# Optimization experiments

Measured on AMD Instinct MI355X. Metric: run time of the kernel, lower is better.

## Reference

```python
import jax, jax.numpy as jnp
import numpy as np
from jax import lax

B, C, H, W = 2, 256, 200, 336
N_ROI = 512
NUM_CLASSES = 81


def setup_inputs() -> dict:
    key = jax.random.key(0)
    ks = jax.random.split(key, 20)
    feat = jax.random.normal(ks[0], (B, C, H, W), dtype=jnp.float32)
    # proposals in feature-map coordinates, x1<x2, y1<y2
    x1 = jax.random.uniform(ks[1], (N_ROI,)) * (0.7 * W)
    y1 = jax.random.uniform(ks[2], (N_ROI,)) * (0.7 * H)
    x2 = jnp.minimum(x1 + 8.0 + jax.random.uniform(ks[3], (N_ROI,)) * (0.29 * W), W - 1.0)
    y2 = jnp.minimum(y1 + 8.0 + jax.random.uniform(ks[4], (N_ROI,)) * (0.29 * H), H - 1.0)
    boxes = jnp.stack([x1, y1, x2, y2], axis=1).astype(jnp.float32)
    batch_idx = jax.random.randint(ks[5], (N_ROI,), 0, B)
    s = 0.02
    def rn(k, shape):
        return s * jax.random.normal(k, shape, dtype=jnp.float32)
    d_in = C * 7 * 7  # 12544
    return {
        'feat': feat, 'boxes': boxes,
        'bw1': rn(ks[6], (d_in, 1024)), 'bw2': rn(ks[7], (1024, 1024)), 'bwo': rn(ks[8], (1024, 4 * NUM_CLASSES)),
        'cw1': rn(ks[9], (d_in, 1024)), 'cw2': rn(ks[10], (1024, 1024)), 'cwo': rn(ks[11], (1024, NUM_CLASSES)),
        'm1': rn(ks[12], (C, C, 3, 3)), 'm2': rn(ks[13], (C, C, 3, 3)),
        'm3': rn(ks[14], (C, C, 3, 3)), 'm4': rn(ks[15], (C, C, 3, 3)),
        'mdc': rn(ks[16], (C, C, 2, 2)),  # IOHW for conv_transpose
        'mpr': rn(ks[17], (NUM_CLASSES, C, 1, 1)),
        'batch_idx': batch_idx,
    }


def roi_align(feat, boxes, batch_idx, out_size, sampling_ratio=2):
    """Bilinear RoIAlign. feat [B,C,H,W], boxes [N,4] (x1,y1,x2,y2) in feature coords.
    Returns [N,C,out_size,out_size]."""
    N = boxes.shape[0]
    _, Cc, Hh, Ww = feat.shape
    P = out_size * sampling_ratio
    x1, y1, x2, y2 = boxes[:, 0], boxes[:, 1], boxes[:, 2], boxes[:, 3]
    steps = (jnp.arange(P, dtype=feat.dtype) + 0.5) / P  # [P]
    xs = jnp.clip(x1[:, None] + steps[None, :] * (x2 - x1)[:, None], 0.0, Ww - 1.0)  # [N,P]
    ys = jnp.clip(y1[:, None] + steps[None, :] * (y2 - y1)[:, None], 0.0, Hh - 1.0)  # [N,P]
    x0 = jnp.floor(xs).astype(jnp.int32); x1i = jnp.minimum(x0 + 1, Ww - 1); lx = xs - x0
    y0 = jnp.floor(ys).astype(jnp.int32); y1i = jnp.minimum(y0 + 1, Hh - 1); ly = ys - y0
    b = batch_idx[:, None, None]                   # [N,1,1]
    yy0, yy1 = y0[:, :, None], y1i[:, :, None]     # [N,P,1]
    xx0, xx1 = x0[:, None, :], x1i[:, None, :]     # [N,1,P]
    # gathers -> [N,P,P,C] (advanced indices first, channel slice last)
    f00 = feat[b, :, yy0, xx0]
    f01 = feat[b, :, yy0, xx1]
    f10 = feat[b, :, yy1, xx0]
    f11 = feat[b, :, yy1, xx1]
    wy = ly[:, :, None, None]  # [N,P,1,1]
    wx = lx[:, None, :, None]  # [N,1,P,1]
    val = (f00 * (1 - wy) * (1 - wx) + f01 * (1 - wy) * wx
           + f10 * wy * (1 - wx) + f11 * wy * wx)  # [N,P,P,C]
    pooled = val.reshape(N, out_size, sampling_ratio, out_size, sampling_ratio, Cc).mean(axis=(2, 4))
    return pooled.transpose(0, 3, 1, 2)  # [N,C,out,out]


def _conv(x, w, pad='SAME'):
    return lax.conv_general_dilated(x, w, (1, 1), pad,
                                    dimension_numbers=('NCHW', 'OIHW', 'NCHW'))


def reference(feat, boxes, bw1, bw2, bwo, cw1, cw2, cwo,
              m1, m2, m3, m4, mdc, mpr, batch_idx):
    # RoIAlign (post-NMS proposals) -> box / cls / mask heads
    r7 = roi_align(feat, boxes, batch_idx, 7, 2)          # [N,C,7,7]
    flat = r7.reshape(r7.shape[0], -1)                    # [N, C*49]
    box_result = jax.nn.relu(jax.nn.relu(flat @ bw1) @ bw2) @ bwo   # [N, 4*classes]
    cls_result = jax.nn.relu(jax.nn.relu(flat @ cw1) @ cw2) @ cwo   # [N, classes]
    x = roi_align(feat, boxes, batch_idx, 14, 2)          # [N,C,14,14]
    for w in (m1, m2, m3, m4):
        x = jax.nn.relu(_conv(x, w))
    x = jax.nn.relu(lax.conv_transpose(x, mdc, (2, 2), 'VALID',
                                       dimension_numbers=('NCHW', 'IOHW', 'NCHW')))  # [N,C,28,28]
    mask_result = _conv(x, mpr)                           # [N, classes, 28, 28]
    return (box_result, cls_result, mask_result)
```

## Files before the change

### kernel.cpp

```cpp
#include <hip/hip_runtime.h>
#include <stdint.h>

#define BB 2
#define CC 256
#define HH 200
#define WW 336
#define NROI 512
#define NCLS 81

typedef __attribute__((ext_vector_type(8))) short bf16x8;
typedef __attribute__((ext_vector_type(4))) float f32x4;

__device__ inline unsigned short f2bf(float f) {
  unsigned int u = __builtin_bit_cast(unsigned int, f);
  u += 0x7fffu + ((u >> 16) & 1u);
  return (unsigned short)(u >> 16);
}
__device__ inline float bf2f(unsigned short h) {
  unsigned int u = ((unsigned int)h) << 16;
  return __builtin_bit_cast(float, u);
}

__device__ inline void gl_lds(const void* gp, void* lp) {
  __builtin_amdgcn_global_load_lds(
      (const __attribute__((address_space(1))) unsigned int*)gp,
      (__attribute__((address_space(3))) unsigned int*)lp, 16, 0, 0);
}

__global__ void k_nchw2nhwc(const float* __restrict__ src, unsigned short* __restrict__ dst) {
  __shared__ float t[32][33];
  int b = blockIdx.z;
  int p0 = blockIdx.x * 32;
  int c0 = blockIdx.y * 32;
  int tx = threadIdx.x & 31, ty = threadIdx.x >> 5;
  const float* s = src + (size_t)b * CC * HH * WW;
  unsigned short* d = dst + (size_t)b * CC * HH * WW;
#pragma unroll
  for (int q = 0; q < 4; ++q)
    t[ty + q * 8][tx] = s[(size_t)(c0 + ty + q * 8) * (HH * WW) + p0 + tx];
  __syncthreads();
#pragma unroll
  for (int q = 0; q < 4; ++q)
    d[(size_t)(p0 + ty + q * 8) * CC + c0 + tx] = f2bf(t[tx][ty + q * 8]);
}

__global__ void k_repack_convw4(const float* __restrict__ w0, const float* __restrict__ w1,
                                const float* __restrict__ w2, const float* __restrict__ w3,
                                unsigned short* __restrict__ wT) {
  int d = blockIdx.x * 256 + threadIdx.x;
  if (d >= 589824) return;
  int which = blockIdx.y;
  const float* w = (which == 0) ? w0 : (which == 1) ? w1 : (which == 2) ? w2 : w3;
  int c = d & 255, o = (d >> 8) & 255, t = d >> 16;
  wT[(size_t)which * 589824 + d] = f2bf(w[o * 2304 + c * 9 + t]);
}

__global__ void k_repack_deconv(const float* __restrict__ mdc, unsigned short* __restrict__ wd) {
  int d = blockIdx.x * 256 + threadIdx.x;
  if (d >= 262144) return;
  int c = d & 255, o = (d >> 8) & 255, tap = d >> 16;
  int r = tap >> 1, s = tap & 1;
  wd[d] = f2bf(mdc[c * 1024 + o * 4 + (1 - r) * 2 + (1 - s)]);
}

__global__ void k_repack_mpr(const float* __restrict__ mpr, unsigned short* __restrict__ mT) {
  int d = blockIdx.x * 256 + threadIdx.x;
  if (d >= 32768) return;
  int c = d & 255, o = d >> 8;
  mT[d] = (o < 81) ? f2bf(mpr[o * 256 + c]) : (unsigned short)0;
}

__global__ void k_repack_w1(const float* __restrict__ src, unsigned short* __restrict__ dst) {
  __shared__ float t[32][33];
  int s = blockIdx.x;
  int c0 = blockIdx.y * 32;
  int n0 = blockIdx.z * 32;
  int tx = threadIdx.x & 31, ty = threadIdx.x >> 5;
#pragma unroll
  for (int q = 0; q < 4; ++q)
    t[ty + q * 8][tx] = src[(size_t)((c0 + ty + q * 8) * 49 + s) * 1024 + n0 + tx];
  __syncthreads();
#pragma unroll
  for (int q = 0; q < 4; ++q)
    dst[(size_t)(n0 + ty + q * 8) * 12544 + s * 256 + c0 + tx] = f2bf(t[tx][ty + q * 8]);
}

__global__ void k_transpose_w(const float* __restrict__ src, unsigned short* __restrict__ dst,
                              int K, int Nreal, int Nphys) {
  __shared__ float t[32][33];
  int k0 = blockIdx.x * 32;
  int n0 = blockIdx.y * 32;
  int tx = threadIdx.x & 31, ty = threadIdx.x >> 5;
#pragma unroll
  for (int q = 0; q < 4; ++q) {
    int n = n0 + tx;
    t[ty + q * 8][tx] = (n < Nreal) ? src[(size_t)(k0 + ty + q * 8) * Nreal + n] : 0.f;
  }
  __syncthreads();
#pragma unroll
  for (int q = 0; q < 4; ++q) {
    int n = n0 + ty + q * 8;
    if (n < Nphys) dst[(size_t)n * K + k0 + tx] = f2bf(t[tx][ty + q * 8]);
  }
}

__global__ void k_zero_border(unsigned short* __restrict__ r14p,
                              unsigned short* __restrict__ cbufA,
                              unsigned short* __restrict__ cbufB) {
  unsigned short* base = (blockIdx.y == 0) ? r14p : (blockIdx.y == 1) ? cbufA : cbufB;
  uint4 z = {0u, 0u, 0u, 0u};
#pragma unroll
  for (int q = 0; q < 8; ++q) {
    int lin = blockIdx.x * 2048 + q * 256 + threadIdx.x;
    int row = lin >> 5, u4 = lin & 31;
    int img = row / 60, b = row - img * 60;
    int y, x;
    if (b < 16) { y = 0; x = b; }
    else if (b < 32) { y = 15; x = b - 16; }
    else { int rem = b - 32; y = 1 + (rem >> 1); x = (rem & 1) * 15; }
    int slot = img * 256 + y * 16 + x;
    ((uint4*)base)[(size_t)slot * 32 + u4] = z;
  }
}

template <int OS>
__global__ void k_roialign(const unsigned short* __restrict__ featN, const float* __restrict__ boxes,
                           const int* __restrict__ bidx, unsigned short* __restrict__ out) {
  const int S = OS * OS;
  int blk = blockIdx.x;
  int n = blk / S;
  int s = blk - n * S;
  int oy = s / OS, ox = s - oy * OS;
  int c = threadIdx.x;
  float x1 = boxes[n * 4 + 0], y1 = boxes[n * 4 + 1];
  float x2 = boxes[n * 4 + 2], y2 = boxes[n * 4 + 3];
  const unsigned short* fb = featN + (size_t)bidx[n] * HH * WW * CC;
  const float P = (float)(OS * 2);
  float acc = 0.f;
#pragma unroll
  for (int sy = 0; sy < 2; ++sy)
#pragma unroll
    for (int sx = 0; sx < 2; ++sx) {
      float xs = x1 + ((float)(ox * 2 + sx) + 0.5f) / P * (x2 - x1);
      float ys = y1 + ((float)(oy * 2 + sy) + 0.5f) / P * (y2 - y1);
      xs = fminf(fmaxf(xs, 0.f), (float)(WW - 1));
      ys = fminf(fmaxf(ys, 0.f), (float)(HH - 1));
      int x0 = (int)floorf(xs);
      int y0 = (int)floorf(ys);
      int x1i = min(x0 + 1, WW - 1);
      int y1i = min(y0 + 1, HH - 1);
      float lx = xs - (float)x0, ly = ys - (float)y0;
      float f00 = bf2f(fb[((y0 * WW + x0) << 8) + c]);
      float f01 = bf2f(fb[((y0 * WW + x1i) << 8) + c]);
      float f10 = bf2f(fb[((y1i * WW + x0) << 8) + c]);
      float f11 = bf2f(fb[((y1i * WW + x1i) << 8) + c]);
      acc += f00 * (1.f - ly) * (1.f - lx) + f01 * (1.f - ly) * lx +
             f10 * ly * (1.f - lx) + f11 * ly * lx;
    }
  acc *= 0.25f;
  if (OS == 7) {
    out[(size_t)n * 12544 + s * 256 + c] = f2bf(acc);
  } else {
    int slot = n * 256 + (oy + 1) * 16 + (ox + 1);
    out[((size_t)slot << 8) + c] = f2bf(acc);
  }
}

#define TM 128
#define TN 128
#define TK 32

__global__ __launch_bounds__(256) void k_gemm_bf16(
    const unsigned short* __restrict__ A0, const unsigned short* __restrict__ Bt0, void* __restrict__ O0p,
    const unsigned short* __restrict__ A1, const unsigned short* __restrict__ Bt1, void* __restrict__ O1p,
    int K, int Nreal, int ldO, int mode, int relu, int ki, int kj) {
  const unsigned short* A = blockIdx.z ? A1 : A0;
  const unsigned short* Bt = blockIdx.z ? Bt1 : Bt0;
  void* Op = blockIdx.z ? O1p : O0p;

  __shared__ unsigned short As[TM * TK];
  __shared__ unsigned short Bs[TN * TK];

  int tid = threadIdx.x, lane = tid & 63, w = tid >> 6;
  int m0 = blockIdx.y * TM, n0 = blockIdx.x * TN;
  int lr = lane >> 2, lc = (lane & 3) * 8;

  const unsigned short* aP[2];
  const unsigned short* bP[2];
  unsigned short* asL[2];
  unsigned short* bsL[2];
#pragma unroll
  for (int s = 0; s < 2; ++s) {
    int seg = w * 2 + s;
    aP[s] = A + (size_t)(m0 + seg * 16 + lr) * K + lc;
    bP[s] = Bt + (size_t)(n0 + seg * 16 + lr) * K + lc;
    asL[s] = As + seg * 512;
    bsL[s] = Bs + seg * 512;
  }

  f32x4 acc[4][4] = {};
  int wm = (w & 1) * 64, wn = (w >> 1) * 64;
  int qa = (lane >> 4) * 8, rl = lane & 15;

  for (int k0 = 0; k0 < K; k0 += TK) {
    gl_lds(aP[0], asL[0]);
    gl_lds(aP[1], asL[1]);
    gl_lds(bP[0], bsL[0]);
    gl_lds(bP[1], bsL[1]);
    aP[0] += TK; aP[1] += TK; bP[0] += TK; bP[1] += TK;
    __syncthreads();
    bf16x8 af[4], bfr[4];
#pragma unroll
    for (int i = 0; i < 4; ++i)
      af[i] = *(const bf16x8*)&As[(wm + i * 16 + rl) * TK + qa];
#pragma unroll
    for (int j = 0; j < 4; ++j)
      bfr[j] = *(const bf16x8*)&Bs[(wn + j * 16 + rl) * TK + qa];
#pragma unroll
    for (int i = 0; i < 4; ++i)
#pragma unroll
      for (int j = 0; j < 4; ++j)
        acc[i][j] = __builtin_amdgcn_mfma_f32_16x16x32_bf16(af[i], bfr[j], acc[i][j], 0, 0, 0);
    __syncthreads();
  }

  int col = lane & 15, rquad = (lane >> 4) * 4;
#pragma unroll
  for (int i = 0; i < 4; ++i) {
#pragma unroll
    for (int j = 0; j < 4; ++j) {
      int gn = n0 + wn + j * 16 + col;
#pragma unroll
      for (int r = 0; r < 4; ++r) {
        int gm = m0 + wm + i * 16 + rquad + r;
        float v = acc[i][j][r];
        if (relu) v = fmaxf(v, 0.f);
        if (mode == 0) {
          ((unsigned short*)Op)[(size_t)gm * ldO + gn] = f2bf(v);
        } else if (mode == 1) {
          if (gn < Nreal) ((float*)Op)[(size_t)gm * ldO + gn] = v;
        } else {
          if (gn < Nreal) {
            int nimg = gm / 196;
            int s2 = gm - nimg * 196;
            int ii = s2 / 14, jj = s2 - ii * 14;
            size_t dst = (((size_t)nimg * 81 + gn) * 28 + (2 * ii + ki)) * 28 + (2 * jj + kj);
            ((float*)Op)[dst] = v;
          }
        }
      }
    }
  }
}

__global__ __launch_bounds__(256) void k_fc1(
    const unsigned short* __restrict__ A, const unsigned short* __restrict__ Bb,
    const unsigned short* __restrict__ Bc, float* __restrict__ Opart) {
  int head = blockIdx.z >> 3, slice = blockIdx.z & 7;
  const unsigned short* Bt = head ? Bc : Bb;

  __shared__ unsigned short As[TM * TK];
  __shared__ unsigned short Bs[TN * TK];

  int tid = threadIdx.x, lane = tid & 63, w = tid >> 6;
  int m0 = blockIdx.y * TM, n0 = blockIdx.x * TN;
  int lr = lane >> 2, lc = (lane & 3) * 8;
  int kbase = slice * 1568;

  const unsigned short* aP[2];
  const unsigned short* bP[2];
  unsigned short* asL[2];
  unsigned short* bsL[2];
#pragma unroll
  for (int s = 0; s < 2; ++s) {
    int seg = w * 2 + s;
    aP[s] = A + (size_t)(m0 + seg * 16 + lr) * 12544 + kbase + lc;
    bP[s] = Bt + (size_t)(n0 + seg * 16 + lr) * 12544 + kbase + lc;
    asL[s] = As + seg * 512;
    bsL[s] = Bs + seg * 512;
  }

  f32x4 acc[4][4] = {};
  int wm = (w & 1) * 64, wn = (w >> 1) * 64;
  int qa = (lane >> 4) * 8, rl = lane & 15;

  for (int k0 = 0; k0 < 1568; k0 += TK) {
    gl_lds(aP[0], asL[0]);
    gl_lds(aP[1], asL[1]);
    gl_lds(bP[0], bsL[0]);
    gl_lds(bP[1], bsL[1]);
    aP[0] += TK; aP[1] += TK; bP[0] += TK; bP[1] += TK;
    __syncthreads();
    bf16x8 af[4], bfr[4];
#pragma unroll
    for (int i = 0; i < 4; ++i)
      af[i] = *(const bf16x8*)&As[(wm + i * 16 + rl) * TK + qa];
#pragma unroll
    for (int j = 0; j < 4; ++j)
      bfr[j] = *(const bf16x8*)&Bs[(wn + j * 16 + rl) * TK + qa];
#pragma unroll
    for (int i = 0; i < 4; ++i)
#pragma unroll
      for (int j = 0; j < 4; ++j)
        acc[i][j] = __builtin_amdgcn_mfma_f32_16x16x32_bf16(af[i], bfr[j], acc[i][j], 0, 0, 0);
    __syncthreads();
  }

  float* O = Opart + (size_t)(head * 8 + slice) * 524288;
  int col = lane & 15, rquad = (lane >> 4) * 4;
#pragma unroll
  for (int i = 0; i < 4; ++i)
#pragma unroll
    for (int j = 0; j < 4; ++j) {
      int gn = n0 + wn + j * 16 + col;
#pragma unroll
      for (int r = 0; r < 4; ++r) {
        int gm = m0 + wm + i * 16 + rquad + r;
        O[(size_t)gm * 1024 + gn] = acc[i][j][r];
      }
    }
}

__global__ void k_fc1red(const float* __restrict__ part, unsigned short* __restrict__ h1b,
                         unsigned short* __restrict__ h1c) {
  int head = blockIdx.y;
  int i = blockIdx.x * 256 + threadIdx.x;
  const float* p = part + (size_t)head * 8 * 524288 + i;
  float s = 0.f;
#pragma unroll
  for (int q = 0; q < 8; ++q) s += p[(size_t)q * 524288];
  unsigned short* h = head ? h1c : h1b;
  h[i] = f2bf(fmaxf(s, 0.f));
}

template <int PADOUT>
__global__ __launch_bounds__(512, 2) void k_conv256(const unsigned short* __restrict__ act,
                                                    const unsigned short* __restrict__ wt,
                                                    unsigned short* __restrict__ out) {
  __shared__ unsigned short As[2][16384];
  __shared__ unsigned short Bs[2][16384];

  int tid = threadIdx.x, lane = tid & 63, wv = tid >> 6;
  int mt = (blockIdx.x & 7) * 49 + (blockIdx.x >> 3);
  int m0 = mt * 256;

  int r8 = tid >> 3;
  int j8 = ((tid & 7) ^ (r8 & 7)) * 8;
  int slotA[4];
  int bElem[4];
#pragma unroll
  for (int q = 0; q < 4; ++q) {
    int row = q * 64 + r8;
    int gm = m0 + row;
    int n = gm / 196;
    int rem = gm - n * 196;
    int y = rem / 14, x = rem - y * 14;
    slotA[q] = n * 256 + (y + 1) * 16 + (x + 1);
    bElem[q] = row * 256 + j8;
  }
  int ldsU = wv * 512;

  int wr = wv >> 2, wc = wv & 3;
  int rl = lane & 15, lg = lane >> 4, e = lane & 7;
  int s0 = (lg ^ e) * 8;
  int s1 = ((4 + lg) ^ e) * 8;
  int rowA = (wr * 128 + rl) * 64;
  int rowB = (wc * 64 + rl) * 64;

  f32x4 acc[8][4] = {};

#define STAGE_A(S, D)                                                             \
  do {                                                                            \
    int cb_ = (S) / 9;                                                            \
    int t_ = (S) - cb_ * 9;                                                       \
    int ky_ = t_ / 3, kx_ = t_ - ky_ * 3;                                         \
    int tapd_ = (ky_ - 1) * 16 + (kx_ - 1);                                       \
    int coff_ = cb_ * 64;                                                         \
    _Pragma("unroll") for (int q = 0; q < 4; ++q)                                 \
        gl_lds(act + (size_t)(slotA[q] + tapd_) * 256 + coff_ + j8,               \
               &As[D][q * 4096 + ldsU]);                                          \
  } while (0)

#define STAGE_B(S, D)                                                             \
  do {                                                                            \
    int cb_ = (S) / 9;                                                            \
    int t_ = (S) - cb_ * 9;                                                       \
    int coff_ = cb_ * 64;                                                         \
    _Pragma("unroll") for (int q = 0; q < 4; ++q)                                 \
        gl_lds(wt + (size_t)t_ * 65536 + bElem[q] + coff_,                        \
               &Bs[D][q * 4096 + ldsU]);                                          \
  } while (0)

#define LOAD_A(QI)                                                                \
  _Pragma("unroll") for (int fi = 0; fi < 4; ++fi) {                              \
    a[fi][0] = *(const bf16x8*)&Ab[rowA + (QI)*4096 + fi * 1024 + s0];            \
    a[fi][1] = *(const bf16x8*)&Ab[rowA + (QI)*4096 + fi * 1024 + s1];            \
  }

#define LOAD_B(QJ, BREG)                                                          \
  _Pragma("unroll") for (int fj = 0; fj < 2; ++fj) {                              \
    BREG[fj][0] = *(const bf16x8*)&Bb[rowB + (QJ)*2048 + fj * 1024 + s0];         \
    BREG[fj][1] = *(const bf16x8*)&Bb[rowB + (QJ)*2048 + fj * 1024 + s1];         \
  }

#define QUAD(QI, QJ, BREG)                                                        \
  __builtin_amdgcn_s_setprio(1);                                                  \
  _Pragma("unroll") for (int fi = 0; fi < 4; ++fi)                                \
  _Pragma("unroll") for (int fj = 0; fj < 2; ++fj) {                              \
    acc[(QI)*4 + fi][(QJ)*2 + fj] = __builtin_amdgcn_mfma_f32_16x16x32_bf16(      \
        a[fi][0], BREG[fj][0], acc[(QI)*4 + fi][(QJ)*2 + fj], 0, 0, 0);           \
    acc[(QI)*4 + fi][(QJ)*2 + fj] = __builtin_amdgcn_mfma_f32_16x16x32_bf16(      \
        a[fi][1], BREG[fj][1], acc[(QI)*4 + fi][(QJ)*2 + fj], 0, 0, 0);           \
  }                                                                               \
  __builtin_amdgcn_s_setprio(0);

  STAGE_A(0, 0);
  STAGE_B(0, 0);

  for (int s = 0; s < 36; ++s) {
    int cur = s & 1, nxt = cur ^ 1;
    const unsigned short* Ab = As[cur];
    const unsigned short* Bb = Bs[cur];
    if (s < 35) {
      STAGE_A(s + 1, nxt);
      asm volatile("s_waitcnt vmcnt(4)" ::: "memory");
    } else {
      asm volatile("s_waitcnt vmcnt(0)" ::: "memory");
    }
    __builtin_amdgcn_s_barrier();
    __builtin_amdgcn_sched_barrier(0);

    bf16x8 a[4][2], b0[2][2], b1[2][2];
    LOAD_A(0);
    LOAD_B(0, b0);
    __builtin_amdgcn_s_barrier();
    QUAD(0, 0, b0);
    __builtin_amdgcn_s_barrier();
    LOAD_B(1, b1);
    if (s < 35) STAGE_B(s + 1, nxt);
    __builtin_amdgcn_s_barrier();
    QUAD(0, 1, b1);
    __builtin_amdgcn_s_barrier();
    LOAD_A(1);
    __builtin_amdgcn_s_barrier();
    QUAD(1, 0, b0);
    __builtin_amdgcn_s_barrier();
    QUAD(1, 1, b1);
    __builtin_amdgcn_s_barrier();
    __builtin_amdgcn_sched_barrier(0);
  }
#undef STAGE_A
#undef STAGE_B
#undef LOAD_A
#undef LOAD_B
#undef QUAD

  int col = lane & 15, rquad = lg * 4;
#pragma unroll
  for (int fi = 0; fi < 8; ++fi) {
#pragma unroll
    for (int r = 0; r < 4; ++r) {
      int gm = m0 + wr * 128 + fi * 16 + rquad + r;
      size_t rowbase;
      if (PADOUT) {
        int n = gm / 196;
        int rem = gm - n * 196;
        int y = rem / 14, x = rem - y * 14;
        rowbase = ((size_t)(n * 256 + (y + 1) * 16 + (x + 1))) << 8;
      } else {
        rowbase = (size_t)gm << 8;
      }
#pragma unroll
      for (int fj = 0; fj < 4; ++fj) {
        int gn = wc * 64 + fj * 16 + col;
        out[rowbase + gn] = f2bf(fmaxf(acc[fi][fj][r], 0.f));
      }
    }
  }
}

extern "C" void kernel_launch(void* const* d_in, const int* in_sizes, int n_in,
                              void* d_out, int out_size, void* d_ws, size_t ws_size,
                              hipStream_t stream) {
  (void)in_sizes; (void)n_in; (void)out_size; (void)ws_size;
  const float* feat = (const float*)d_in[0];
  const float* boxes = (const float*)d_in[1];
  const float* bw1 = (const float*)d_in[2];
  const float* bw2 = (const float*)d_in[3];
  const float* bwo = (const float*)d_in[4];
  const float* cw1 = (const float*)d_in[5];
  const float* cw2 = (const float*)d_in[6];
  const float* cwo = (const float*)d_in[7];
  const float* m1 = (const float*)d_in[8];
  const float* m2 = (const float*)d_in[9];
  const float* m3 = (const float*)d_in[10];
  const float* m4 = (const float*)d_in[11];
  const float* mdc = (const float*)d_in[12];
  const float* mpr = (const float*)d_in[13];
  const int* bidx = (const int*)d_in[14];

  char* p = (char*)d_ws;
  unsigned short* featN = (unsigned short*)p; p += 68812800;
  unsigned short* cbufA = featN;
  unsigned short* cbufB = (unsigned short*)p; p += 67108864;
  float* fc1part = (float*)cbufB;
  unsigned short* r14p = (unsigned short*)p;  p += 67108864;
  unsigned short* dflat = (unsigned short*)p; p += 51380224;
  unsigned short* ddec = (unsigned short*)p;  p += 51380224;
  unsigned short* r7b = (unsigned short*)p;   p += 12845056;
  unsigned short* h1b = (unsigned short*)p;   p += 1048576;
  unsigned short* h1c = (unsigned short*)p;   p += 1048576;
  unsigned short* h2b = (unsigned short*)p;   p += 1048576;
  unsigned short* h2c = (unsigned short*)p;   p += 1048576;
  unsigned short* wTb = (unsigned short*)p;   p += 4718592;
  unsigned short* wdb = (unsigned short*)p;   p += 524288;
  unsigned short* mprTb = (unsigned short*)p; p += 65536;
  unsigned short* bw1b = (unsigned short*)p;  p += 25690112;
  unsigned short* cw1b = (unsigned short*)p;  p += 25690112;
  unsigned short* bw2b = (unsigned short*)p;  p += 2097152;
  unsigned short* cw2b = (unsigned short*)p;  p += 2097152;
  unsigned short* bwob = (unsigned short*)p;  p += 786432;
  unsigned short* cwob = (unsigned short*)p;  p += 262144;

  float* outBox = (float*)d_out;
  float* outCls = outBox + 512 * 324;
  float* outMask = outCls + 512 * 81;

  k_nchw2nhwc<<<dim3(2100, 8, 2), 256, 0, stream>>>(feat, featN);
  k_repack_convw4<<<dim3(2304, 4), 256, 0, stream>>>(m1, m2, m3, m4, wTb);
  k_repack_deconv<<<dim3(1024), 256, 0, stream>>>(mdc, wdb);
  k_repack_mpr<<<dim3(128), 256, 0, stream>>>(mpr, mprTb);
  k_repack_w1<<<dim3(49, 8, 32), 256, 0, stream>>>(bw1, bw1b);
  k_repack_w1<<<dim3(49, 8, 32), 256, 0, stream>>>(cw1, cw1b);
  k_transpose_w<<<dim3(32, 32), 256, 0, stream>>>(bw2, bw2b, 1024, 1024, 1024);
  k_transpose_w<<<dim3(32, 32), 256, 0, stream>>>(cw2, cw2b, 1024, 1024, 1024);
  k_transpose_w<<<dim3(32, 12), 256, 0, stream>>>(bwo, bwob, 1024, 324, 384);
  k_transpose_w<<<dim3(32, 4), 256, 0, stream>>>(cwo, cwob, 1024, 81, 128);

  k_roialign<7><<<dim3(512 * 49), 256, 0, stream>>>(featN, boxes, bidx, r7b);
  k_roialign<14><<<dim3(512 * 196), 256, 0, stream>>>(featN, boxes, bidx, r14p);

  k_fc1<<<dim3(8, 4, 16), 256, 0, stream>>>(r7b, bw1b, cw1b, fc1part);
  k_fc1red<<<dim3(2048, 2), 256, 0, stream>>>(fc1part, h1b, h1c);
  k_gemm_bf16<<<dim3(8, 4, 2), 256, 0, stream>>>(h1b, bw2b, h2b, h1c, cw2b, h2c,
                                                 1024, 1024, 1024, 0, 1, 0, 0);
  k_gemm_bf16<<<dim3(3, 4, 1), 256, 0, stream>>>(h2b, bwob, outBox, h2b, bwob, outBox,
                                                 1024, 324, 324, 1, 0, 0, 0);
  k_gemm_bf16<<<dim3(1, 4, 1), 256, 0, stream>>>(h2c, cwob, outCls, h2c, cwob, outCls,
                                                 1024, 81, 81, 1, 0, 0, 0);

  k_zero_border<<<dim3(480, 3), 256, 0, stream>>>(r14p, cbufA, cbufB);
  k_conv256<1><<<dim3(392), 512, 0, stream>>>(r14p, wTb + 0 * 589824, cbufA);
  k_conv256<1><<<dim3(392), 512, 0, stream>>>(cbufA, wTb + 1 * 589824, cbufB);
  k_conv256<1><<<dim3(392), 512, 0, stream>>>(cbufB, wTb + 2 * 589824, cbufA);
  k_conv256<0><<<dim3(392), 512, 0, stream>>>(cbufA, wTb + 3 * 589824, dflat);

  for (int r = 0; r < 2; ++r)
    for (int s = 0; s < 2; ++s) {
      int tap = r * 2 + s;
      k_gemm_bf16<<<dim3(2, 784, 1), 256, 0, stream>>>(
          dflat, wdb + tap * 65536, ddec, dflat, wdb, ddec,
          256, 256, 256, 0, 1, 0, 0);
      k_gemm_bf16<<<dim3(1, 784, 1), 256, 0, stream>>>(
          ddec, mprTb, outMask, ddec, mprTb, outMask,
          256, 81, 0, 2, 0, r, s);
    }
}
```

Baseline: 1.651 ms.

## Fuse deconv taps and mask predictor into one LDS-resident mask-head kernel

Replaces the eight launches (four deconv-tap GEMMs that write ddec to global, each followed by a predictor GEMM) with a single kernel. Each block loads a 128-row tile of dflat into swizzled LDS once, computes each deconv tap with MFMA into LDS, applies ReLU, then runs the 81-class 1x1 predictor from LDS and scatters results into the 28x28 mask output. This removes the round trips of the large intermediate through global memory, the repeated dflat reads and the launch overhead. In exchange it uses 128KB of LDS per block, which limits occupancy, reads weights straight from global without staging, and writes the output with scattered stores.

```diff
diff --git a/kernel.cpp b/kernel.cpp
--- a/kernel.cpp
+++ b/kernel.cpp
@@ -479,6 +479,113 @@
   }
 }
 
+__global__ __launch_bounds__(512) void k_maskhead(const unsigned short* __restrict__ dflat,
+                                                  const unsigned short* __restrict__ wdb,
+                                                  const unsigned short* __restrict__ mprTb,
+                                                  float* __restrict__ outMask) {
+  __shared__ unsigned short Xs[32768];
+  __shared__ unsigned short Ms[32768];
+
+  int tid = threadIdx.x, lane = tid & 63, wv = tid >> 6;
+  int m0 = blockIdx.x * 128;
+
+#pragma unroll
+  for (int q = 0; q < 8; ++q) {
+    int lin = q * 512 + tid;
+    int row = lin >> 5, c = lin & 31;
+    int csrc = (c & 24) | ((c & 7) ^ (row & 7));
+    gl_lds(dflat + (size_t)(m0 + row) * 256 + csrc * 8,
+           &Xs[(q * 512 + wv * 64) * 8]);
+  }
+  asm volatile("s_waitcnt vmcnt(0)" ::: "memory");
+  __syncthreads();
+
+  int wr2 = wv >> 2, wc2 = wv & 3;
+  int rl = lane & 15, lg = lane >> 4;
+
+  for (int tap = 0; tap < 4; ++tap) {
+    const unsigned short* Wt = wdb + tap * 65536;
+    f32x4 acc[4][4] = {};
+#pragma unroll
+    for (int ks = 0; ks < 8; ++ks) {
+      int clog = lg + ks * 4;
+      bf16x8 a[4], b[4];
+#pragma unroll
+      for (int fi = 0; fi < 4; ++fi) {
+        int row = wr2 * 64 + fi * 16 + rl;
+        int cp = (clog & 24) | ((clog & 7) ^ (row & 7));
+        a[fi] = *(const bf16x8*)&Xs[row * 256 + cp * 8];
+      }
+#pragma unroll
+      for (int j = 0; j < 4; ++j) {
+        int n = wc2 * 64 + j * 16 + rl;
+        b[j] = *(const bf16x8*)&Wt[(size_t)n * 256 + clog * 8];
+      }
+      __builtin_amdgcn_s_setprio(1);
+#pragma unroll
+      for (int fi = 0; fi < 4; ++fi)
+#pragma unroll
+        for (int j = 0; j < 4; ++j)
+          acc[fi][j] = __builtin_amdgcn_mfma_f32_16x16x32_bf16(a[fi], b[j], acc[fi][j], 0, 0, 0);
+      __builtin_amdgcn_s_setprio(0);
+    }
+#pragma unroll
+    for (int fi = 0; fi < 4; ++fi)
+#pragma unroll
+      for (int j = 0; j < 4; ++j)
+#pragma unroll
+        for (int r = 0; r < 4; ++r) {
+          int row = wr2 * 64 + fi * 16 + lg * 4 + r;
+          int col = wc2 * 64 + j * 16 + rl;
+          Ms[row * 256 + (col ^ ((row & 7) << 3))] = f2bf(fmaxf(acc[fi][j][r], 0.f));
+        }
+    __syncthreads();
+    f32x4 acc2[4][2] = {};
+#pragma unroll
+    for (int ks = 0; ks < 8; ++ks) {
+      int clog = lg + ks * 4;
+      bf16x8 a[4], b[2];
+#pragma unroll
+      for (int fi = 0; fi < 4; ++fi) {
+        int row = wr2 * 64 + fi * 16 + rl;
+        int cp = (clog & 24) | ((clog & 7) ^ (row & 7));
+        a[fi] = *(const bf16x8*)&Ms[row * 256 + cp * 8];
+      }
+#pragma unroll
+      for (int j = 0; j < 2; ++j) {
+        int o = wc2 * 32 + j * 16 + rl;
+        b[j] = *(const bf16x8*)&mprTb[(size_t)o * 256 + clog * 8];
+      }
+      __builtin_amdgcn_s_setprio(1);
+#pragma unroll
+      for (int fi = 0; fi < 4; ++fi)
+#pragma unroll
+        for (int j = 0; j < 2; ++j)
+          acc2[fi][j] = __builtin_amdgcn_mfma_f32_16x16x32_bf16(a[fi], b[j], acc2[fi][j], 0, 0, 0);
+      __builtin_amdgcn_s_setprio(0);
+    }
+    int tr = tap >> 1, tc = tap & 1;
+#pragma unroll
+    for (int fi = 0; fi < 4; ++fi)
+#pragma unroll
+      for (int j = 0; j < 2; ++j) {
+        int o = wc2 * 32 + j * 16 + rl;
+        if (o < 81) {
+#pragma unroll
+          for (int r = 0; r < 4; ++r) {
+            int gm = m0 + wr2 * 64 + fi * 16 + lg * 4 + r;
+            int nimg = gm / 196;
+            int s2 = gm - nimg * 196;
+            int ii = s2 / 14, jj = s2 - ii * 14;
+            size_t dst = (((size_t)nimg * 81 + o) * 28 + (2 * ii + tr)) * 28 + (2 * jj + tc);
+            outMask[dst] = acc2[fi][j][r];
+          }
+        }
+      }
+    __syncthreads();
+  }
+}
+
 extern "C" void kernel_launch(void* const* d_in, const int* in_sizes, int n_in,
                               void* d_out, int out_size, void* d_ws, size_t ws_size,
                               hipStream_t stream) {
@@ -521,6 +628,7 @@
   unsigned short* cw2b = (unsigned short*)p;  p += 2097152;
   unsigned short* bwob = (unsigned short*)p;  p += 786432;
   unsigned short* cwob = (unsigned short*)p;  p += 262144;
+  (void)ddec;
 
   float* outBox = (float*)d_out;
   float* outCls = outBox + 512 * 324;
@@ -555,14 +663,5 @@
   k_conv256<1><<<dim3(392), 512, 0, stream>>>(cbufB, wTb + 2 * 589824, cbufA);
   k_conv256<0><<<dim3(392), 512, 0, stream>>>(cbufA, wTb + 3 * 589824, dflat);
 
-  for (int r = 0; r < 2; ++r)
-    for (int s = 0; s < 2; ++s) {
-      int tap = r * 2 + s;
-      k_gemm_bf16<<<dim3(2, 784, 1), 256, 0, stream>>>(
-          dflat, wdb + tap * 65536, ddec, dflat, wdb, ddec,
-          256, 256, 256, 0, 1, 0, 0);
-      k_gemm_bf16<<<dim3(1, 784, 1), 256, 0, stream>>>(
-          ddec, mprTb, outMask, ddec, mprTb, outMask,
-          256, 81, 0, 2, 0, r, s);
-    }
-}
+  k_maskhead<<<dim3(784), 512, 0, stream>>>(dflat, wdb, mprTb, outMask);
+}
```

After: 1.864 ms. 12.9% more time.
